# Optimization experiments

Hardware: AMD Instinct MI355X
Metric: run time of the kernel (lower is better)

## Reference

```python
import jax, jax.numpy as jnp
import numpy as np
from math import sqrt

B, S, F, H, FF, L = 16, 512, 512, 8, 2048, 3
HEAD_DIM = F // H
LN_EPS = 1e-5


def setup_inputs() -> dict:
    key = jax.random.key(0)
    ks = iter(jax.random.split(key, 80))

    def nrm(shape, scale=0.02):
        return jax.random.normal(next(ks), shape, jnp.float32) * scale

    inp = {
        "embedding": jax.random.normal(next(ks), (B, S, F), jnp.float32),
        "lengths": jax.random.randint(next(ks), (B,), 1, S + 1, dtype=jnp.int32),
    }
    for p in ("enc", "dec"):
        inp[p + "_wqkv"] = nrm((L, 3, F, F))
        inp[p + "_bqkv"] = nrm((L, 3, F))
        inp[p + "_wo"] = nrm((L, F, F))
        inp[p + "_bo"] = nrm((L, F))
        inp[p + "_ln1_g"] = jnp.ones((L, F), jnp.float32)
        inp[p + "_ln1_b"] = jnp.zeros((L, F), jnp.float32)
        inp[p + "_ff_w1"] = nrm((L, F, FF))
        inp[p + "_ff_b1"] = nrm((L, FF))
        inp[p + "_ff_w2"] = nrm((L, FF, F))
        inp[p + "_ff_b2"] = nrm((L, F))
        inp[p + "_ln2_g"] = jnp.ones((L, F), jnp.float32)
        inp[p + "_ln2_b"] = jnp.zeros((L, F), jnp.float32)
    inp["ptr_w_q"] = nrm((F,), 1.0)
    inp["ptr_w_k"] = nrm((F,), 1.0)
    return inp


def _ln(x, g, b):
    mu = x.mean(-1, keepdims=True)
    var = ((x - mu) ** 2).mean(-1, keepdims=True)
    return (x - mu) / jnp.sqrt(var + LN_EPS) * g + b


def _mha(q_in, kv_in, wqkv, bqkv, wo, bo, mask):
    # q_in [b,sq,f], kv_in [b,sk,f], mask broadcastable to [b,h,sq,sk] (True = masked)
    b, sq, f = q_in.shape
    q = q_in @ wqkv[0] + bqkv[0]
    k = kv_in @ wqkv[1] + bqkv[1]
    v = kv_in @ wqkv[2] + bqkv[2]

    def split(t):
        return t.reshape(t.shape[0], t.shape[1], H, HEAD_DIM).transpose(0, 2, 1, 3)

    q, k, v = split(q), split(k), split(v)  # [b,h,s,dh]
    scores = jnp.einsum("bhqd,bhkd->bhqk", q, k) / sqrt(HEAD_DIM)
    scores = jnp.where(mask, jnp.finfo(scores.dtype).min, scores)
    attn = jax.nn.softmax(scores, axis=-1)
    out = jnp.einsum("bhqk,bhkd->bhqd", attn, v)
    out = out.transpose(0, 2, 1, 3).reshape(b, sq, f)
    return out @ wo + bo


def _layer(x, mem, mask, wqkv, bqkv, wo, bo, ln1_g, ln1_b, w1, b1, w2, b2, ln2_g, ln2_b):
    x = _ln(x + _mha(x, mem, wqkv, bqkv, wo, bo, mask), ln1_g, ln1_b)
    ff = jax.nn.gelu(x @ w1 + b1, approximate=False) @ w2 + b2
    return _ln(x + ff, ln2_g, ln2_b)


def _forward(embedding, lengths,
             enc_wqkv, enc_bqkv, enc_wo, enc_bo, enc_ln1_g, enc_ln1_b,
             enc_ff_w1, enc_ff_b1, enc_ff_w2, enc_ff_b2, enc_ln2_g, enc_ln2_b,
             dec_wqkv, dec_bqkv, dec_wo, dec_bo, dec_ln1_g, dec_ln1_b,
             dec_ff_w1, dec_ff_b1, dec_ff_w2, dec_ff_b2, dec_ln2_g, dec_ln2_b,
             ptr_w_q, ptr_w_k):
    b, s, f = embedding.shape
    pos = jnp.arange(s)
    key_mask = pos[None, :] >= lengths[:, None]  # [b,s] True = padded

    # ---- encoder (self-attn with key padding mask) ----
    enc_mask = key_mask[:, None, None, :]  # [b,1,1,s]
    x = embedding
    for i in range(L):
        x = _layer(x, x, enc_mask,
                   enc_wqkv[i], enc_bqkv[i], enc_wo[i], enc_bo[i],
                   enc_ln1_g[i], enc_ln1_b[i],
                   enc_ff_w1[i], enc_ff_b1[i], enc_ff_w2[i], enc_ff_b2[i],
                   enc_ln2_g[i], enc_ln2_b[i])
    memory = x

    # ---- decoder: all timesteps batched (no recurrent state in original loop) ----
    # query t attends keys j < min(t, len); t=0 is overridden with zeros below
    # (key 0 left unmasked for t=0 only to keep softmax finite).
    t = jnp.arange(s)
    limit = jnp.minimum(jnp.maximum(t, 1)[None, :], lengths[:, None])  # [b,sq]
    dec_mask = (pos[None, None, :] >= limit[:, :, None])[:, None, :, :]  # [b,1,sq,sk]
    y = embedding
    for i in range(L):
        y = _layer(y, memory, dec_mask,
                   dec_wqkv[i], dec_bqkv[i], dec_wo[i], dec_bo[i],
                   dec_ln1_g[i], dec_ln1_b[i],
                   dec_ff_w1[i], dec_ff_b1[i], dec_ff_w2[i], dec_ff_b2[i],
                   dec_ln2_g[i], dec_ln2_b[i])

    # ---- pointer logits ----
    wq = y @ ptr_w_q        # [b, sq]
    wk = memory @ ptr_w_k   # [b, sk]
    ptr = jax.nn.sigmoid((wq[:, None, :] + wk[:, :, None]) / sqrt(f))  # [b, sk, sq]
    return jnp.where(t[None, None, :] == 0, 0.0, ptr)


def reference(embedding, lengths,
              enc_wqkv, enc_bqkv, enc_wo, enc_bo, enc_ln1_g, enc_ln1_b,
              enc_ff_w1, enc_ff_b1, enc_ff_w2, enc_ff_b2, enc_ln2_g, enc_ln2_b,
              dec_wqkv, dec_bqkv, dec_wo, dec_bo, dec_ln1_g, dec_ln1_b,
              dec_ff_w1, dec_ff_b1, dec_ff_w2, dec_ff_b2, dec_ln2_g, dec_ln2_b,
              ptr_w_q, ptr_w_k):
    return _forward(embedding, lengths,
                    enc_wqkv, enc_bqkv, enc_wo, enc_bo, enc_ln1_g, enc_ln1_b,
                    enc_ff_w1, enc_ff_b1, enc_ff_w2, enc_ff_b2, enc_ln2_g, enc_ln2_b,
                    dec_wqkv, dec_bqkv, dec_wo, dec_bo, dec_ln1_g, dec_ln1_b,
                    dec_ff_w1, dec_ff_b1, dec_ff_w2, dec_ff_b2, dec_ln2_g, dec_ln2_b,
                    ptr_w_q, ptr_w_k)
```

## Files before the change

### kernel.cpp

```cpp
#include <hip/hip_runtime.h>
#include <hip/hip_bf16.h>
#include <math.h>

#define TB 16
#define TS 512
#define TF 512
#define TH 8
#define TFF 2048
#define TL 3

typedef unsigned short u16;
typedef short bf16x8 __attribute__((ext_vector_type(8)));
typedef float f32x4 __attribute__((ext_vector_type(4)));

__device__ __forceinline__ u16 f2b(float f) {
    __hip_bfloat16 h = __float2bfloat16(f);
    return *reinterpret_cast<u16*>(&h);
}
__device__ __forceinline__ float b2f(u16 u) {
    unsigned int v = ((unsigned int)u) << 16;
    return __builtin_bit_cast(float, v);
}

__device__ __forceinline__ void gload_lds16(const void* g, void* l) {
    __builtin_amdgcn_global_load_lds(
        (const __attribute__((address_space(1))) unsigned int*)g,
        (__attribute__((address_space(3))) unsigned int*)l, 16, 0, 0);
}

__global__ __launch_bounds__(256) void k_transpose_w(
    const float* __restrict__ src, u16* __restrict__ dst, int K, int N)
{
    __shared__ float tile[32][33];
    const int z = blockIdx.z;
    src += (size_t)z * K * N;
    dst += (size_t)z * K * N;
    const int n0 = blockIdx.x * 32, k0 = blockIdx.y * 32;
    const int tx = threadIdx.x & 31, ty = threadIdx.x >> 5;
    #pragma unroll
    for (int i = 0; i < 32; i += 8)
        tile[ty + i][tx] = src[(size_t)(k0 + ty + i) * N + n0 + tx];
    __syncthreads();
    #pragma unroll
    for (int i = 0; i < 32; i += 8)
        dst[(size_t)(n0 + ty + i) * K + k0 + tx] = f2b(tile[tx][ty + i]);
}

__global__ __launch_bounds__(256) void k_cvt(
    const float* __restrict__ src, u16* __restrict__ d16, int n4)
{
    const int i = blockIdx.x * 256 + threadIdx.x;
    if (i >= n4) return;
    float4 v = ((const float4*)src)[i];
    ushort4 p;
    p.x = f2b(v.x); p.y = f2b(v.y); p.z = f2b(v.z); p.w = f2b(v.w);
    ((ushort4*)d16)[i] = p;
}

template<int EPI, int BM, int BN>
__global__ __launch_bounds__(512, 2) void k_g8(
    const u16* __restrict__ A, const u16* __restrict__ A2, int asplit,
    const u16* __restrict__ BT,
    const float* __restrict__ bias, const u16* __restrict__ residb,
    u16* __restrict__ outb,
    u16* __restrict__ out_k, u16* __restrict__ out_v,
    int N, int K, int ldo, int coloff)
{
    constexpr int WN  = (BM == 256) ? 2 : 4;
    constexpr int CS  = BN / WN;
    constexpr int NFB = CS / 16;
    constexpr int NLA = BM / 64, NLB = BN / 64;
    constexpr int NL  = NLA + NLB;
    __shared__ __align__(16) u16 SH[2 * BM * 64 + 2 * BN * 64];
    u16* Asm = SH;
    u16* Bsm = SH + 2 * BM * 64;

    const int gx = gridDim.x;
    int bid = blockIdx.y * gx + blockIdx.x;
    const int cpx = (gx * gridDim.y) >> 3;
    bid = (bid & 7) * cpx + (bid >> 3);
    const int bn = bid % gx, bm = bid / gx;

    const int t = threadIdx.x;
    const int w = t >> 6, l = t & 63;
    const int wm = w / WN, wn = w % WN;
    const int lhi = l >> 4, llo = l & 15;

    f32x4 acc[4][NFB];
    #pragma unroll
    for (int m = 0; m < 4; ++m)
        #pragma unroll
        for (int n = 0; n < NFB; ++n)
            acc[m][n] = f32x4{0.f, 0.f, 0.f, 0.f};

    const u16* Asrc = (bn * BN < asplit) ? A : A2;
    const int lr = l >> 3;
    const int lcz = ((l & 7) ^ lr) * 8;
    const u16* Ag = Asrc + (size_t)(bm * BM + w * 8 + lr) * K + lcz;
    const u16* Bg = BT + (size_t)(bn * BN + w * 8 + lr) * K + lcz;

    auto stage = [&](int buf, int tt) {
        const int kofs = tt << 6;
        #pragma unroll
        for (int i = 0; i < NLA; ++i)
            gload_lds16(Ag + (size_t)i * 64 * K + kofs,
                        Asm + buf * (BM * 64) + (i * 64 + w * 8) * 64);
        #pragma unroll
        for (int i = 0; i < NLB; ++i)
            gload_lds16(Bg + (size_t)i * 64 * K + kofs,
                        Bsm + buf * (BN * 64) + (i * 64 + w * 8) * 64);
    };

    const int NT = K >> 6;
    stage(0, 0);
    stage(1, 1);
    for (int tt = 0; tt < NT; ++tt) {
        const int cur = tt & 1;
        if (tt + 1 < NT) {
            if constexpr (NL == 8) asm volatile("s_waitcnt vmcnt(8)" ::: "memory");
            else                   asm volatile("s_waitcnt vmcnt(4)" ::: "memory");
        } else {
            asm volatile("s_waitcnt vmcnt(0)" ::: "memory");
        }
        __builtin_amdgcn_s_barrier();
        __builtin_amdgcn_sched_barrier(0);

        const u16* Ab = Asm + cur * (BM * 64);
        const u16* Bb = Bsm + cur * (BN * 64);
        bf16x8 af[4][2], bfr[NFB][2];
        #pragma unroll
        for (int m = 0; m < 4; ++m) {
            const int row = wm * 64 + m * 16 + llo;
            const int x = row & 7;
            af[m][0] = *(const bf16x8*)(Ab + row * 64 + ((lhi) ^ x) * 8);
            af[m][1] = *(const bf16x8*)(Ab + row * 64 + ((4 + lhi) ^ x) * 8);
        }
        #pragma unroll
        for (int n = 0; n < NFB; ++n) {
            const int row = wn * CS + n * 16 + llo;
            const int x = row & 7;
            bfr[n][0] = *(const bf16x8*)(Bb + row * 64 + ((lhi) ^ x) * 8);
            bfr[n][1] = *(const bf16x8*)(Bb + row * 64 + ((4 + lhi) ^ x) * 8);
        }
        asm volatile("s_waitcnt lgkmcnt(0)" ::: "memory");
        __builtin_amdgcn_sched_barrier(0);
        __builtin_amdgcn_s_barrier();
        if (tt + 2 < NT) stage(cur, tt + 2);
        __builtin_amdgcn_s_setprio(1);
        #pragma unroll
        for (int kk = 0; kk < 2; ++kk)
            #pragma unroll
            for (int m = 0; m < 4; ++m)
                #pragma unroll
                for (int n = 0; n < NFB; ++n)
                    acc[m][n] = __builtin_amdgcn_mfma_f32_16x16x32_bf16(
                        af[m][kk], bfr[n][kk], acc[m][n], 0, 0, 0);
        __builtin_amdgcn_s_setprio(0);
        __builtin_amdgcn_sched_barrier(0);
    }

    const int colb = bn * BN + wn * CS;
    const int rowb = bm * BM + wm * 64 + lhi * 4;
    const int c0w = coloff + colb;

    if constexpr (EPI == 3 && BM == 256) {
        if (c0w >= 1024) {
            __builtin_amdgcn_s_barrier();
            u16* tb = SH + w * 8192;
            #pragma unroll
            for (int nh = 0; nh < 2; ++nh) {
                #pragma unroll
                for (int ni = 0; ni < 4; ++ni) {
                    const int n = nh * 4 + ni;
                    const int dl = ni * 16 + llo;
                    const float bv = bias[colb + n * 16 + llo];
                    #pragma unroll
                    for (int m = 0; m < 4; ++m) {
                        ushort4 pk;
                        #pragma unroll
                        for (int r = 0; r < 4; ++r)
                            ((u16*)&pk)[r] = f2b(acc[m][n][r] + bv);
                        const int slc = m * 2 + (lhi >> 1);
                        const int addr = nh * 4096 + dl * 64
                                       + ((slc ^ (dl & 7)) << 3) + ((lhi & 1) << 2);
                        *(ushort4*)(tb + addr) = pk;
                    }
                }
            }
            asm volatile("s_waitcnt lgkmcnt(0)" ::: "memory");
            __builtin_amdgcn_sched_barrier(0);
            const int sbase = bm * BM + wm * 64;
            const int bidx = sbase >> 9;
            const int srem = sbase & 511;
            const int cchunk = l & 7;
            #pragma unroll
            for (int nh = 0; nh < 2; ++nh) {
                const int hh = (((c0w >> 6) + nh) & 7);
                u16* vo = out_v + ((size_t)bidx * 8 + hh) * 32768 + srem;
                #pragma unroll
                for (int rr = 0; rr < 8; ++rr) {
                    const int dl2 = (l >> 3) + rr * 8;
                    const int ch = cchunk ^ (dl2 & 7);
                    bf16x8 vv = *(const bf16x8*)(tb + nh * 4096 + dl2 * 64 + ch * 8);
                    *(bf16x8*)(vo + (size_t)dl2 * 512 + cchunk * 8) = vv;
                }
            }
            return;
        }
    }

    #pragma unroll
    for (int n = 0; n < NFB; ++n) {
        const int col = colb + n * 16 + llo;
        const float bv = bias[col];
        #pragma unroll
        for (int m = 0; m < 4; ++m) {
            const int row = rowb + m * 16;
            if (EPI == 3) {
                float vv[4];
                #pragma unroll
                for (int r = 0; r < 4; ++r) vv[r] = acc[m][n][r] + bv;
                const int c = coloff + col;
                if ((c >> 9) == 0) {
                    #pragma unroll
                    for (int r = 0; r < 4; ++r)
                        outb[(size_t)(row + r) * 512 + c] = f2b(vv[r]);
                } else {
                    const int hh = (c >> 6) & 7, d = c & 63;
                    #pragma unroll
                    for (int r = 0; r < 4; ++r) {
                        const int rr = row + r;
                        out_k[((size_t)(rr >> 9) * 8 + hh) * 32768 + (rr & 511) * 64 + d] = f2b(vv[r]);
                    }
                }
            } else {
                #pragma unroll
                for (int r = 0; r < 4; ++r) {
                    float v = acc[m][n][r] + bv;
                    const size_t off = (size_t)(row + r) * ldo + coloff + col;
                    if (EPI == 0) {
                        outb[off] = f2b(v);
                    } else if (EPI == 1) {
                        v = 0.5f * v * (1.f + erff(v * 0.70710678118654752f));
                        outb[off] = f2b(v);
                    } else {
                        v += b2f(residb[off]);
                        outb[off] = f2b(v);
                    }
                }
            }
        }
    }
}

template<int DEC>
__global__ __launch_bounds__(256) void k_attn(
    const u16* __restrict__ qb, const u16* __restrict__ kc,
    const u16* __restrict__ vtp, const int* __restrict__ lengths,
    u16* __restrict__ out)
{
    __shared__ __align__(16) u16 Ks[2][64 * 64];
    __shared__ __align__(16) u16 Vs[2][64 * 64];
    __shared__ __align__(16) u16 plds[4][16][64];
    __shared__ float alds[4][16];
    __shared__ float llds[4][16];
    const int qt = blockIdx.x;
    const int bh = blockIdx.y;
    const int b = bh >> 3;
    const int h = bh & 7;
    const int t = threadIdx.x, w = t >> 6, l = t & 63;
    const int lhi = l >> 4, llo = l & 15;
    const int len = lengths[b];
    const int qrow0 = qt * 64 + w * 16;
    const int q = qrow0 + llo;

    const u16* qp = qb + (size_t)(b * TS + q) * 512 + h * 64 + lhi * 8;
    bf16x8 qf0 = *(const bf16x8*)(qp);
    bf16x8 qf1 = *(const bf16x8*)(qp + 32);

    const u16* kb = kc  + (size_t)bh * 32768;
    const u16* vb = vtp + (size_t)bh * 32768;

    const int qlim = DEC ? min(max(q, 1), len) : len;
    const int limb = DEC ? min(qt * 64 + 63, len) : len;
    const int ktend = (limb + 63) >> 6;

    f32x4 o[4];
    #pragma unroll
    for (int g = 0; g < 4; ++g) o[g] = f32x4{0.f, 0.f, 0.f, 0.f};
    float mrun = -1e30f, lrun = 0.f;

    const float SC = 0.18033688011112042f;

    const int sr = w * 8 + (l >> 3);
    const int sc = (((l & 7) ^ (sr & 7)) << 3);
    auto stage = [&](int buf, int ktt) {
        gload_lds16(kb + ((ktt * 64 + sr) << 6) + sc,        &Ks[buf][(w * 8) * 64]);
        gload_lds16(kb + ((ktt * 64 + 32 + sr) << 6) + sc,   &Ks[buf][(32 + w * 8) * 64]);
        gload_lds16(vb + (size_t)sr * 512 + ktt * 64 + sc,   &Vs[buf][(w * 8) * 64]);
        gload_lds16(vb + (size_t)(32 + sr) * 512 + ktt * 64 + sc, &Vs[buf][(32 + w * 8) * 64]);
    };

    stage(0, 0);
    for (int kt = 0; kt < ktend; ++kt) {
        const int cur = kt & 1;
        if (kt + 1 < ktend) {
            stage(cur ^ 1, kt + 1);
            asm volatile("s_waitcnt vmcnt(4)" ::: "memory");
        } else {
            asm volatile("s_waitcnt vmcnt(0)" ::: "memory");
        }
        __builtin_amdgcn_s_barrier();
        __builtin_amdgcn_sched_barrier(0);

        bf16x8 kf[4][2], vf[4][2];
        #pragma unroll
        for (int g = 0; g < 4; ++g) {
            const int row = g * 16 + llo;
            const int x = row & 7;
            kf[g][0] = *(const bf16x8*)&Ks[cur][row * 64 + ((lhi) ^ x) * 8];
            kf[g][1] = *(const bf16x8*)&Ks[cur][row * 64 + ((4 + lhi) ^ x) * 8];
            vf[g][0] = *(const bf16x8*)&Vs[cur][row * 64 + ((lhi) ^ x) * 8];
            vf[g][1] = *(const bf16x8*)&Vs[cur][row * 64 + ((4 + lhi) ^ x) * 8];
        }
        f32x4 s[4];
        #pragma unroll
        for (int g = 0; g < 4; ++g) {
            s[g] = f32x4{0.f, 0.f, 0.f, 0.f};
            s[g] = __builtin_amdgcn_mfma_f32_16x16x32_bf16(kf[g][0], qf0, s[g], 0, 0, 0);
            s[g] = __builtin_amdgcn_mfma_f32_16x16x32_bf16(kf[g][1], qf1, s[g], 0, 0, 0);
        }
        #pragma unroll
        for (int g = 0; g < 4; ++g) {
            const int key = kt * 64 + g * 16 + lhi * 4;
            #pragma unroll
            for (int r = 0; r < 4; ++r)
                s[g][r] = (key + r < qlim) ? s[g][r] * SC : -1e30f;
        }
        float tm = fmaxf(fmaxf(fmaxf(s[0][0], s[0][1]), fmaxf(s[0][2], s[0][3])),
                         fmaxf(fmaxf(s[1][0], s[1][1]), fmaxf(s[1][2], s[1][3])));
        tm = fmaxf(tm, fmaxf(fmaxf(fmaxf(s[2][0], s[2][1]), fmaxf(s[2][2], s[2][3])),
                             fmaxf(fmaxf(s[3][0], s[3][1]), fmaxf(s[3][2], s[3][3]))));
        tm = fmaxf(tm, __shfl_xor(tm, 16));
        tm = fmaxf(tm, __shfl_xor(tm, 32));
        const float mnew = fmaxf(mrun, tm);
        const float alpha = exp2f(mrun - mnew);
        mrun = mnew;
        float rs = 0.f;
        ushort4 pk[4];
        #pragma unroll
        for (int g = 0; g < 4; ++g) {
            #pragma unroll
            for (int r = 0; r < 4; ++r) {
                const float p = exp2f(s[g][r] - mnew);
                rs += p;
                ((u16*)&pk[g])[r] = f2b(p);
            }
        }
        rs += __shfl_xor(rs, 16);
        rs += __shfl_xor(rs, 32);
        lrun = lrun * alpha + rs;
        if (lhi == 0) alds[w][llo] = alpha;
        #pragma unroll
        for (int g = 0; g < 4; ++g) {
            const int chw = (g * 2 + (lhi >> 1)) ^ (llo & 7);
            *(ushort4*)((char*)&plds[w][0][0] + llo * 128 + chw * 16 + (lhi & 1) * 8) = pk[g];
        }
        const float4 av = *(const float4*)&alds[w][lhi * 4];
        #pragma unroll
        for (int g = 0; g < 4; ++g) {
            o[g][0] *= av.x; o[g][1] *= av.y; o[g][2] *= av.z; o[g][3] *= av.w;
        }
        #pragma unroll
        for (int ks = 0; ks < 2; ++ks) {
            const int chr = (ks * 4 + lhi) ^ (llo & 7);
            bf16x8 pa = *(const bf16x8*)((const char*)&plds[w][0][0] + llo * 128 + chr * 16);
            #pragma unroll
            for (int g = 0; g < 4; ++g)
                o[g] = __builtin_amdgcn_mfma_f32_16x16x32_bf16(pa, vf[g][ks], o[g], 0, 0, 0);
        }
        __builtin_amdgcn_sched_barrier(0);
        __builtin_amdgcn_s_barrier();
    }

    if (lhi == 0) llds[w][llo] = 1.f / lrun;
    __builtin_amdgcn_s_waitcnt(0);
    const float4 linv = *(const float4*)&llds[w][lhi * 4];
    #pragma unroll
    for (int g = 0; g < 4; ++g) {
        const int d = h * 64 + g * 16 + llo;
        #pragma unroll
        for (int r = 0; r < 4; ++r) {
            const int qq = qrow0 + lhi * 4 + r;
            out[(size_t)(b * TS + qq) * 512 + d] = f2b(o[g][r] * ((const float*)&linv)[r]);
        }
    }
}

__global__ __launch_bounds__(256) void k_ln(
    const u16* __restrict__ in, const float* __restrict__ gam,
    const float* __restrict__ bet, u16* __restrict__ o16,
    const float* __restrict__ dotv, float* __restrict__ dotout)
{
    const int row = blockIdx.x * 4 + (threadIdx.x >> 6);
    const int l = threadIdx.x & 63;
    bf16x8 vin = *(const bf16x8*)(in + (size_t)row * 512 + l * 8);
    float x[8];
    #pragma unroll
    for (int i = 0; i < 8; ++i) x[i] = b2f((u16)vin[i]);
    float s = x[0] + x[1] + x[2] + x[3] + x[4] + x[5] + x[6] + x[7];
    #pragma unroll
    for (int off = 32; off; off >>= 1) s += __shfl_xor(s, off);
    const float mu = s * (1.f / 512.f);
    float v = 0.f;
    #pragma unroll
    for (int i = 0; i < 8; ++i) { const float d = x[i] - mu; v += d * d; }
    #pragma unroll
    for (int off = 32; off; off >>= 1) v += __shfl_xor(v, off);
    const float rstd = rsqrtf(v * (1.f / 512.f) + 1e-5f);
    float gg[8], bb[8];
    *(float4*)&gg[0] = *(const float4*)(gam + l * 8);
    *(float4*)&gg[4] = *(const float4*)(gam + l * 8 + 4);
    *(float4*)&bb[0] = *(const float4*)(bet + l * 8);
    *(float4*)&bb[4] = *(const float4*)(bet + l * 8 + 4);
    float y[8];
    #pragma unroll
    for (int i = 0; i < 8; ++i) y[i] = (x[i] - mu) * rstd * gg[i] + bb[i];
    ushort4 pk0, pk1;
    pk0.x = f2b(y[0]); pk0.y = f2b(y[1]); pk0.z = f2b(y[2]); pk0.w = f2b(y[3]);
    pk1.x = f2b(y[4]); pk1.y = f2b(y[5]); pk1.z = f2b(y[6]); pk1.w = f2b(y[7]);
    ushort4* o16p = (ushort4*)(o16 + (size_t)row * 512 + l * 8);
    o16p[0] = pk0; o16p[1] = pk1;
    if (dotv) {
        float wa[8];
        *(float4*)&wa[0] = *(const float4*)(dotv + l * 8);
        *(float4*)&wa[4] = *(const float4*)(dotv + l * 8 + 4);
        float ds = 0.f;
        #pragma unroll
        for (int i = 0; i < 8; ++i) ds += y[i] * wa[i];
        #pragma unroll
        for (int off = 32; off; off >>= 1) ds += __shfl_xor(ds, off);
        if (l == 0) dotout[row] = ds;
    }
}

__global__ __launch_bounds__(256) void k_ptr_out(
    const float* __restrict__ wq, const float* __restrict__ wk, float* __restrict__ out)
{
    const int bi = blockIdx.x;
    const int b = bi >> 9;
    const float wki = wk[bi];
    #pragma unroll
    for (int j = threadIdx.x; j < 512; j += 256) {
        float r = 0.f;
        if (j != 0) {
            const float z = (wq[b * 512 + j] + wki) * 0.044194173824159216f;
            r = 1.f / (1.f + __expf(-z));
        }
        out[(size_t)bi * 512 + j] = r;
    }
}

extern "C" void kernel_launch(void* const* d_in, const int* in_sizes, int n_in,
                              void* d_out, int out_size, void* d_ws, size_t ws_size,
                              hipStream_t stream)
{
    const float* emb = (const float*)d_in[0];
    const int* lengths = (const int*)d_in[1];
    struct Pw {
        const float *wqkv, *bqkv, *wo, *bo, *ln1g, *ln1b, *w1, *b1, *w2, *b2, *ln2g, *ln2b;
    } pp[2];
    for (int p = 0; p < 2; ++p) {
        const int base = 2 + p * 12;
        pp[p].wqkv = (const float*)d_in[base + 0];
        pp[p].bqkv = (const float*)d_in[base + 1];
        pp[p].wo   = (const float*)d_in[base + 2];
        pp[p].bo   = (const float*)d_in[base + 3];
        pp[p].ln1g = (const float*)d_in[base + 4];
        pp[p].ln1b = (const float*)d_in[base + 5];
        pp[p].w1   = (const float*)d_in[base + 6];
        pp[p].b1   = (const float*)d_in[base + 7];
        pp[p].w2   = (const float*)d_in[base + 8];
        pp[p].b2   = (const float*)d_in[base + 9];
        pp[p].ln2g = (const float*)d_in[base + 10];
        pp[p].ln2b = (const float*)d_in[base + 11];
    }
    const float* pwq = (const float*)d_in[26];
    const float* pwk = (const float*)d_in[27];

    char* ws = (char*)d_ws;
    auto alloc = [&](size_t bytes) {
        char* p = ws;
        ws += (bytes + 255) & ~(size_t)255;
        return p;
    };
    u16* wqkvT[2], *woT[2], *w1T[2], *w2T[2];
    for (int p = 0; p < 2; ++p) {
        wqkvT[p] = (u16*)alloc((size_t)TL * 1536 * 512 * 2);
        woT[p]   = (u16*)alloc((size_t)TL * 512 * 512 * 2);
        w1T[p]   = (u16*)alloc((size_t)TL * 2048 * 512 * 2);
        w2T[p]   = (u16*)alloc((size_t)TL * 512 * 2048 * 2);
    }
    const size_t MR = (size_t)TB * TS;
    u16*   emb16 = (u16*)alloc(MR * 512 * 2);
    u16*   x16   = (u16*)alloc(MR * 512 * 2);
    u16*   mem16 = (u16*)alloc(MR * 512 * 2);
    u16*   pre16 = (u16*)alloc(MR * 512 * 2);
    u16*   qbuf  = (u16*)alloc(MR * 512 * 2);
    u16*   kcb   = (u16*)alloc((size_t)TB * TH * 512 * 64 * 2);
    u16*   vtb   = (u16*)alloc((size_t)TB * TH * 64 * 512 * 2);
    u16*   att16 = (u16*)alloc(MR * 512 * 2);
    u16*   h16   = (u16*)alloc(MR * 2048 * 2);
    float* wqb   = (float*)alloc(MR * 4);
    float* wkb   = (float*)alloc(MR * 4);

    for (int p = 0; p < 2; ++p) {
        k_transpose_w<<<dim3(16, 16, 9), 256, 0, stream>>>(pp[p].wqkv, wqkvT[p], 512, 512);
        k_transpose_w<<<dim3(16, 16, 3), 256, 0, stream>>>(pp[p].wo, woT[p], 512, 512);
        k_transpose_w<<<dim3(64, 16, 3), 256, 0, stream>>>(pp[p].w1, w1T[p], 512, 2048);
        k_transpose_w<<<dim3(16, 64, 3), 256, 0, stream>>>(pp[p].w2, w2T[p], 2048, 512);
    }

    const int n4 = (int)(MR * 512 / 4);
    k_cvt<<<4096, 256, 0, stream>>>(emb, emb16, n4);

    for (int i = 0; i < TL; ++i) {
        const u16* xin = (i == 0) ? emb16 : x16;
        k_g8<3, 256, 256><<<dim3(6, 32), 512, 0, stream>>>(
            xin, xin, 1536, wqkvT[0] + (size_t)i * 1536 * 512, pp[0].bqkv + i * 1536,
            nullptr, qbuf, kcb, vtb, 1536, 512, 1536, 0);
        k_attn<0><<<dim3(8, 128), 256, 0, stream>>>(qbuf, kcb, vtb, lengths, att16);
        k_g8<2, 128, 128><<<dim3(4, 64), 512, 0, stream>>>(
            att16, att16, 512, woT[0] + (size_t)i * 512 * 512, pp[0].bo + i * 512,
            xin, pre16, nullptr, nullptr, 512, 512, 512, 0);
        k_ln<<<2048, 256, 0, stream>>>(pre16, pp[0].ln1g + i * 512, pp[0].ln1b + i * 512,
                                       x16, nullptr, nullptr);
        k_g8<1, 256, 256><<<dim3(8, 32), 512, 0, stream>>>(
            x16, x16, 2048, w1T[0] + (size_t)i * 2048 * 512, pp[0].b1 + i * 2048,
            nullptr, h16, nullptr, nullptr, 2048, 512, 2048, 0);
        k_g8<2, 128, 128><<<dim3(4, 64), 512, 0, stream>>>(
            h16, h16, 512, w2T[0] + (size_t)i * 512 * 2048, pp[0].b2 + i * 512,
            x16, pre16, nullptr, nullptr, 512, 2048, 512, 0);
        if (i == TL - 1)
            k_ln<<<2048, 256, 0, stream>>>(pre16, pp[0].ln2g + i * 512, pp[0].ln2b + i * 512,
                                           mem16, pwk, wkb);
        else
            k_ln<<<2048, 256, 0, stream>>>(pre16, pp[0].ln2g + i * 512, pp[0].ln2b + i * 512,
                                           x16, nullptr, nullptr);
    }

    for (int i = 0; i < TL; ++i) {
        const u16* yin = (i == 0) ? emb16 : x16;
        k_g8<3, 256, 256><<<dim3(6, 32), 512, 0, stream>>>(
            yin, mem16, 512, wqkvT[1] + (size_t)i * 1536 * 512, pp[1].bqkv + i * 1536,
            nullptr, qbuf, kcb, vtb, 1536, 512, 1536, 0);
        k_attn<1><<<dim3(8, 128), 256, 0, stream>>>(qbuf, kcb, vtb, lengths, att16);
        k_g8<2, 128, 128><<<dim3(4, 64), 512, 0, stream>>>(
            att16, att16, 512, woT[1] + (size_t)i * 512 * 512, pp[1].bo + i * 512,
            yin, pre16, nullptr, nullptr, 512, 512, 512, 0);
        k_ln<<<2048, 256, 0, stream>>>(pre16, pp[1].ln1g + i * 512, pp[1].ln1b + i * 512,
                                       x16, nullptr, nullptr);
        k_g8<1, 256, 256><<<dim3(8, 32), 512, 0, stream>>>(
            x16, x16, 2048, w1T[1] + (size_t)i * 2048 * 512, pp[1].b1 + i * 2048,
            nullptr, h16, nullptr, nullptr, 2048, 512, 2048, 0);
        k_g8<2, 128, 128><<<dim3(4, 64), 512, 0, stream>>>(
            h16, h16, 512, w2T[1] + (size_t)i * 512 * 2048, pp[1].b2 + i * 512,
            x16, pre16, nullptr, nullptr, 512, 2048, 512, 0);
        if (i == TL - 1)
            k_ln<<<2048, 256, 0, stream>>>(pre16, pp[1].ln2g + i * 512, pp[1].ln2b + i * 512,
                                           x16, pwq, wqb);
        else
            k_ln<<<2048, 256, 0, stream>>>(pre16, pp[1].ln2g + i * 512, pp[1].ln2b + i * 512,
                                           x16, nullptr, nullptr);
    }

    k_ptr_out<<<TB * TS, 256, 0, stream>>>(wqb, wkb, (float*)d_out);
}
```

Before: 836.5 us.

## Add K=512 GEMM kernel with full A panel resident in LDS

Adds a new GEMM kernel k_gp for the K=512 projections (QKV, output projection, FF1). Each block loads an entire 128x512 A panel into LDS once and streams B fragments straight from global memory into registers, with no double-buffered staging or per-step barriers. This targets the per-k-tile barrier and LDS staging overhead. In exchange, B is read without LDS reuse across waves, occupancy drops to one block per CU, and the global-load latency of B is no longer hidden by an async pipeline.

```diff
diff --git a/kernel.cpp b/kernel.cpp
--- a/kernel.cpp
+++ b/kernel.cpp
@@ -57,23 +57,19 @@
     ((ushort4*)d16)[i] = p;
 }
 
-template<int EPI, int BM, int BN>
-__global__ __launch_bounds__(512, 2) void k_g8(
+template<int EPI, int BN>
+__global__ __launch_bounds__(512, 1) void k_gp(
     const u16* __restrict__ A, const u16* __restrict__ A2, int asplit,
     const u16* __restrict__ BT,
     const float* __restrict__ bias, const u16* __restrict__ residb,
     u16* __restrict__ outb,
     u16* __restrict__ out_k, u16* __restrict__ out_v,
-    int N, int K, int ldo, int coloff)
-{
-    constexpr int WN  = (BM == 256) ? 2 : 4;
-    constexpr int CS  = BN / WN;
+    int N, int ldo, int coloff)
+{
+    constexpr int K = 512;
+    constexpr int CS = BN / 4;
     constexpr int NFB = CS / 16;
-    constexpr int NLA = BM / 64, NLB = BN / 64;
-    constexpr int NL  = NLA + NLB;
-    __shared__ __align__(16) u16 SH[2 * BM * 64 + 2 * BN * 64];
-    u16* Asm = SH;
-    u16* Bsm = SH + 2 * BM * 64;
+    __shared__ __align__(16) u16 Asm[128 * 512];
 
     const int gx = gridDim.x;
     int bid = blockIdx.y * gx + blockIdx.x;
@@ -83,8 +79,20 @@
 
     const int t = threadIdx.x;
     const int w = t >> 6, l = t & 63;
-    const int wm = w / WN, wn = w % WN;
+    const int wm = w >> 2, wn = w & 3;
     const int lhi = l >> 4, llo = l & 15;
+
+    const u16* Asrc = (bn * BN < asplit) ? A : A2;
+    const u16* Ablk = Asrc + (size_t)(bm * 128) * K;
+
+    #pragma unroll
+    for (int j = 0; j < 16; ++j) {
+        const int row = w * 16 + j;
+        const int sch = l ^ (row & 7);
+        gload_lds16(Ablk + (size_t)row * K + sch * 8, Asm + row * 512);
+    }
+    asm volatile("s_waitcnt vmcnt(0)" ::: "memory");
+    __syncthreads();
 
     f32x4 acc[4][NFB];
     #pragma unroll
@@ -93,60 +101,27 @@
         for (int n = 0; n < NFB; ++n)
             acc[m][n] = f32x4{0.f, 0.f, 0.f, 0.f};
 
-    const u16* Asrc = (bn * BN < asplit) ? A : A2;
-    const int lr = l >> 3;
-    const int lcz = ((l & 7) ^ lr) * 8;
-    const u16* Ag = Asrc + (size_t)(bm * BM + w * 8 + lr) * K + lcz;
-    const u16* Bg = BT + (size_t)(bn * BN + w * 8 + lr) * K + lcz;
-
-    auto stage = [&](int buf, int tt) {
-        const int kofs = tt << 6;
-        #pragma unroll
-        for (int i = 0; i < NLA; ++i)
-            gload_lds16(Ag + (size_t)i * 64 * K + kofs,
-                        Asm + buf * (BM * 64) + (i * 64 + w * 8) * 64);
-        #pragma unroll
-        for (int i = 0; i < NLB; ++i)
-            gload_lds16(Bg + (size_t)i * 64 * K + kofs,
-                        Bsm + buf * (BN * 64) + (i * 64 + w * 8) * 64);
-    };
-
-    const int NT = K >> 6;
-    stage(0, 0);
-    stage(1, 1);
-    for (int tt = 0; tt < NT; ++tt) {
-        const int cur = tt & 1;
-        if (tt + 1 < NT) {
-            if constexpr (NL == 8) asm volatile("s_waitcnt vmcnt(8)" ::: "memory");
-            else                   asm volatile("s_waitcnt vmcnt(4)" ::: "memory");
-        } else {
-            asm volatile("s_waitcnt vmcnt(0)" ::: "memory");
-        }
-        __builtin_amdgcn_s_barrier();
-        __builtin_amdgcn_sched_barrier(0);
-
-        const u16* Ab = Asm + cur * (BM * 64);
-        const u16* Bb = Bsm + cur * (BN * 64);
-        bf16x8 af[4][2], bfr[NFB][2];
+    const int colb = bn * BN + wn * CS;
+    const u16* Bbase = BT + (size_t)(colb + llo) * K + lhi * 8;
+
+    #pragma unroll 2
+    for (int tt = 0; tt < 8; ++tt) {
+        bf16x8 bfr[NFB][2];
+        #pragma unroll
+        for (int n = 0; n < NFB; ++n) {
+            const u16* bp = Bbase + (size_t)(n * 16) * K + tt * 64;
+            bfr[n][0] = *(const bf16x8*)(bp);
+            bfr[n][1] = *(const bf16x8*)(bp + 32);
+        }
+        bf16x8 af[4][2];
         #pragma unroll
         for (int m = 0; m < 4; ++m) {
             const int row = wm * 64 + m * 16 + llo;
             const int x = row & 7;
-            af[m][0] = *(const bf16x8*)(Ab + row * 64 + ((lhi) ^ x) * 8);
-            af[m][1] = *(const bf16x8*)(Ab + row * 64 + ((4 + lhi) ^ x) * 8);
-        }
-        #pragma unroll
-        for (int n = 0; n < NFB; ++n) {
-            const int row = wn * CS + n * 16 + llo;
-            const int x = row & 7;
-            bfr[n][0] = *(const bf16x8*)(Bb + row * 64 + ((lhi) ^ x) * 8);
-            bfr[n][1] = *(const bf16x8*)(Bb + row * 64 + ((4 + lhi) ^ x) * 8);
-        }
-        asm volatile("s_waitcnt lgkmcnt(0)" ::: "memory");
-        __builtin_amdgcn_sched_barrier(0);
-        __builtin_amdgcn_s_barrier();
-        if (tt + 2 < NT) stage(cur, tt + 2);
-        __builtin_amdgcn_s_setprio(1);
+            const int c0 = tt * 8 + lhi;
+            af[m][0] = *(const bf16x8*)(Asm + row * 512 + ((c0) ^ x) * 8);
+            af[m][1] = *(const bf16x8*)(Asm + row * 512 + ((c0 + 4) ^ x) * 8);
+        }
         #pragma unroll
         for (int kk = 0; kk < 2; ++kk)
             #pragma unroll
@@ -155,55 +130,44 @@
                 for (int n = 0; n < NFB; ++n)
                     acc[m][n] = __builtin_amdgcn_mfma_f32_16x16x32_bf16(
                         af[m][kk], bfr[n][kk], acc[m][n], 0, 0, 0);
-        __builtin_amdgcn_s_setprio(0);
-        __builtin_amdgcn_sched_barrier(0);
-    }
-
-    const int colb = bn * BN + wn * CS;
-    const int rowb = bm * BM + wm * 64 + lhi * 4;
+    }
+
+    const int rowb = bm * 128 + wm * 64 + lhi * 4;
     const int c0w = coloff + colb;
 
-    if constexpr (EPI == 3 && BM == 256) {
+    if constexpr (EPI == 3 && BN == 256) {
         if (c0w >= 1024) {
-            __builtin_amdgcn_s_barrier();
-            u16* tb = SH + w * 8192;
-            #pragma unroll
-            for (int nh = 0; nh < 2; ++nh) {
+            __syncthreads();
+            u16* tb = Asm + w * 4096;
+            #pragma unroll
+            for (int n = 0; n < 4; ++n) {
+                const int dl = n * 16 + llo;
+                const float bv = bias[colb + n * 16 + llo];
                 #pragma unroll
-                for (int ni = 0; ni < 4; ++ni) {
-                    const int n = nh * 4 + ni;
-                    const int dl = ni * 16 + llo;
-                    const float bv = bias[colb + n * 16 + llo];
+                for (int m = 0; m < 4; ++m) {
+                    ushort4 pk;
                     #pragma unroll
-                    for (int m = 0; m < 4; ++m) {
-                        ushort4 pk;
-                        #pragma unroll
-                        for (int r = 0; r < 4; ++r)
-                            ((u16*)&pk)[r] = f2b(acc[m][n][r] + bv);
-                        const int slc = m * 2 + (lhi >> 1);
-                        const int addr = nh * 4096 + dl * 64
-                                       + ((slc ^ (dl & 7)) << 3) + ((lhi & 1) << 2);
-                        *(ushort4*)(tb + addr) = pk;
-                    }
+                    for (int r = 0; r < 4; ++r)
+                        ((u16*)&pk)[r] = f2b(acc[m][n][r] + bv);
+                    const int slc = m * 2 + (lhi >> 1);
+                    const int addr = dl * 64 + ((slc ^ (dl & 7)) << 3) + ((lhi & 1) << 2);
+                    *(ushort4*)(tb + addr) = pk;
                 }
             }
             asm volatile("s_waitcnt lgkmcnt(0)" ::: "memory");
             __builtin_amdgcn_sched_barrier(0);
-            const int sbase = bm * BM + wm * 64;
+            const int sbase = bm * 128 + wm * 64;
             const int bidx = sbase >> 9;
             const int srem = sbase & 511;
+            const int hh = (c0w >> 6) & 7;
+            u16* vo = out_v + ((size_t)bidx * 8 + hh) * 32768 + srem;
             const int cchunk = l & 7;
             #pragma unroll
-            for (int nh = 0; nh < 2; ++nh) {
-                const int hh = (((c0w >> 6) + nh) & 7);
-                u16* vo = out_v + ((size_t)bidx * 8 + hh) * 32768 + srem;
-                #pragma unroll
-                for (int rr = 0; rr < 8; ++rr) {
-                    const int dl2 = (l >> 3) + rr * 8;
-                    const int ch = cchunk ^ (dl2 & 7);
-                    bf16x8 vv = *(const bf16x8*)(tb + nh * 4096 + dl2 * 64 + ch * 8);
-                    *(bf16x8*)(vo + (size_t)dl2 * 512 + cchunk * 8) = vv;
-                }
+            for (int rr = 0; rr < 8; ++rr) {
+                const int dl2 = (l >> 3) + rr * 8;
+                const int ch = cchunk ^ (dl2 & 7);
+                bf16x8 vv = *(const bf16x8*)(tb + dl2 * 64 + ch * 8);
+                *(bf16x8*)(vo + (size_t)dl2 * 512 + cchunk * 8) = vv;
             }
             return;
         }
@@ -238,15 +202,140 @@
                 for (int r = 0; r < 4; ++r) {
                     float v = acc[m][n][r] + bv;
                     const size_t off = (size_t)(row + r) * ldo + coloff + col;
-                    if (EPI == 0) {
-                        outb[off] = f2b(v);
-                    } else if (EPI == 1) {
+                    if (EPI == 1) {
                         v = 0.5f * v * (1.f + erff(v * 0.70710678118654752f));
                         outb[off] = f2b(v);
                     } else {
                         v += b2f(residb[off]);
                         outb[off] = f2b(v);
                     }
+                }
+            }
+        }
+    }
+}
+
+template<int EPI, int BM, int BN>
+__global__ __launch_bounds__(512, 2) void k_g8(
+    const u16* __restrict__ A, const u16* __restrict__ A2, int asplit,
+    const u16* __restrict__ BT,
+    const float* __restrict__ bias, const u16* __restrict__ residb,
+    u16* __restrict__ outb,
+    u16* __restrict__ out_k, u16* __restrict__ out_v,
+    int N, int K, int ldo, int coloff)
+{
+    constexpr int WN  = (BM == 256) ? 2 : 4;
+    constexpr int CS  = BN / WN;
+    constexpr int NFB = CS / 16;
+    constexpr int NLA = BM / 64, NLB = BN / 64;
+    constexpr int NL  = NLA + NLB;
+    __shared__ __align__(16) u16 SH[2 * BM * 64 + 2 * BN * 64];
+    u16* Asm = SH;
+    u16* Bsm = SH + 2 * BM * 64;
+
+    const int gx = gridDim.x;
+    int bid = blockIdx.y * gx + blockIdx.x;
+    const int cpx = (gx * gridDim.y) >> 3;
+    bid = (bid & 7) * cpx + (bid >> 3);
+    const int bn = bid % gx, bm = bid / gx;
+
+    const int t = threadIdx.x;
+    const int w = t >> 6, l = t & 63;
+    const int wm = w / WN, wn = w % WN;
+    const int lhi = l >> 4, llo = l & 15;
+
+    f32x4 acc[4][NFB];
+    #pragma unroll
+    for (int m = 0; m < 4; ++m)
+        #pragma unroll
+        for (int n = 0; n < NFB; ++n)
+            acc[m][n] = f32x4{0.f, 0.f, 0.f, 0.f};
+
+    const u16* Asrc = (bn * BN < asplit) ? A : A2;
+    const int lr = l >> 3;
+    const int lcz = ((l & 7) ^ lr) * 8;
+    const u16* Ag = Asrc + (size_t)(bm * BM + w * 8 + lr) * K + lcz;
+    const u16* Bg = BT + (size_t)(bn * BN + w * 8 + lr) * K + lcz;
+
+    auto stage = [&](int buf, int tt) {
+        const int kofs = tt << 6;
+        #pragma unroll
+        for (int i = 0; i < NLA; ++i)
+            gload_lds16(Ag + (size_t)i * 64 * K + kofs,
+                        Asm + buf * (BM * 64) + (i * 64 + w * 8) * 64);
+        #pragma unroll
+        for (int i = 0; i < NLB; ++i)
+            gload_lds16(Bg + (size_t)i * 64 * K + kofs,
+                        Bsm + buf * (BN * 64) + (i * 64 + w * 8) * 64);
+    };
+
+    const int NT = K >> 6;
+    stage(0, 0);
+    stage(1, 1);
+    for (int tt = 0; tt < NT; ++tt) {
+        const int cur = tt & 1;
+        if (tt + 1 < NT) {
+            if constexpr (NL == 8) asm volatile("s_waitcnt vmcnt(8)" ::: "memory");
+            else                   asm volatile("s_waitcnt vmcnt(4)" ::: "memory");
+        } else {
+            asm volatile("s_waitcnt vmcnt(0)" ::: "memory");
+        }
+        __builtin_amdgcn_s_barrier();
+        __builtin_amdgcn_sched_barrier(0);
+
+        const u16* Ab = Asm + cur * (BM * 64);
+        const u16* Bb = Bsm + cur * (BN * 64);
+        bf16x8 af[4][2], bfr[NFB][2];
+        #pragma unroll
+        for (int m = 0; m < 4; ++m) {
+            const int row = wm * 64 + m * 16 + llo;
+            const int x = row & 7;
+            af[m][0] = *(const bf16x8*)(Ab + row * 64 + ((lhi) ^ x) * 8);
+            af[m][1] = *(const bf16x8*)(Ab + row * 64 + ((4 + lhi) ^ x) * 8);
+        }
+        #pragma unroll
+        for (int n = 0; n < NFB; ++n) {
+            const int row = wn * CS + n * 16 + llo;
+            const int x = row & 7;
+            bfr[n][0] = *(const bf16x8*)(Bb + row * 64 + ((lhi) ^ x) * 8);
+            bfr[n][1] = *(const bf16x8*)(Bb + row * 64 + ((4 + lhi) ^ x) * 8);
+        }
+        asm volatile("s_waitcnt lgkmcnt(0)" ::: "memory");
+        __builtin_amdgcn_sched_barrier(0);
+        __builtin_amdgcn_s_barrier();
+        if (tt + 2 < NT) stage(cur, tt + 2);
+        __builtin_amdgcn_s_setprio(1);
+        #pragma unroll
+        for (int kk = 0; kk < 2; ++kk)
+            #pragma unroll
+            for (int m = 0; m < 4; ++m)
+                #pragma unroll
+                for (int n = 0; n < NFB; ++n)
+                    acc[m][n] = __builtin_amdgcn_mfma_f32_16x16x32_bf16(
+                        af[m][kk], bfr[n][kk], acc[m][n], 0, 0, 0);
+        __builtin_amdgcn_s_setprio(0);
+        __builtin_amdgcn_sched_barrier(0);
+    }
+
+    const int colb = bn * BN + wn * CS;
+    const int rowb = bm * BM + wm * 64 + lhi * 4;
+    #pragma unroll
+    for (int n = 0; n < NFB; ++n) {
+        const int col = colb + n * 16 + llo;
+        const float bv = bias[col];
+        #pragma unroll
+        for (int m = 0; m < 4; ++m) {
+            const int row = rowb + m * 16;
+            #pragma unroll
+            for (int r = 0; r < 4; ++r) {
+                float v = acc[m][n][r] + bv;
+                const size_t off = (size_t)(row + r) * ldo + coloff + col;
+                if (EPI == 1) {
+                    v = 0.5f * v * (1.f + erff(v * 0.70710678118654752f));
+                    outb[off] = f2b(v);
+                } else {
+                    v += b2f(residb[off]);
+                    outb[off] = f2b(v);
                 }
             }
         }
@@ -526,18 +615,18 @@
 
     for (int i = 0; i < TL; ++i) {
         const u16* xin = (i == 0) ? emb16 : x16;
-        k_g8<3, 256, 256><<<dim3(6, 32), 512, 0, stream>>>(
+        k_gp<3, 256><<<dim3(6, 64), 512, 0, stream>>>(
             xin, xin, 1536, wqkvT[0] + (size_t)i * 1536 * 512, pp[0].bqkv + i * 1536,
-            nullptr, qbuf, kcb, vtb, 1536, 512, 1536, 0);
+            nullptr, qbuf, kcb, vtb, 1536, 1536, 0);
         k_attn<0><<<dim3(8, 128), 256, 0, stream>>>(qbuf, kcb, vtb, lengths, att16);
-        k_g8<2, 128, 128><<<dim3(4, 64), 512, 0, stream>>>(
+        k_gp<2, 128><<<dim3(4, 64), 512, 0, stream>>>(
             att16, att16, 512, woT[0] + (size_t)i * 512 * 512, pp[0].bo + i * 512,
-            xin, pre16, nullptr, nullptr, 512, 512, 512, 0);
+            xin, pre16, nullptr, nullptr, 512, 512, 0);
         k_ln<<<2048, 256, 0, stream>>>(pre16, pp[0].ln1g + i * 512, pp[0].ln1b + i * 512,
                                        x16, nullptr, nullptr);
-        k_g8<1, 256, 256><<<dim3(8, 32), 512, 0, stream>>>(
+        k_gp<1, 256><<<dim3(8, 64), 512, 0, stream>>>(
             x16, x16, 2048, w1T[0] + (size_t)i * 2048 * 512, pp[0].b1 + i * 2048,
-            nullptr, h16, nullptr, nullptr, 2048, 512, 2048, 0);
+            nullptr, h16, nullptr, nullptr, 2048, 2048, 0);
         k_g8<2, 128, 128><<<dim3(4, 64), 512, 0, stream>>>(
             h16, h16, 512, w2T[0] + (size_t)i * 512 * 2048, pp[0].b2 + i * 512,
             x16, pre16, nullptr, nullptr, 512, 2048, 512, 0);
@@ -551,18 +640,18 @@
 
     for (int i = 0; i < TL; ++i) {
         const u16* yin = (i == 0) ? emb16 : x16;
-        k_g8<3, 256, 256><<<dim3(6, 32), 512, 0, stream>>>(
+        k_gp<3, 256><<<dim3(6, 64), 512, 0, stream>>>(
             yin, mem16, 512, wqkvT[1] + (size_t)i * 1536 * 512, pp[1].bqkv + i * 1536,
-            nullptr, qbuf, kcb, vtb, 1536, 512, 1536, 0);
+            nullptr, qbuf, kcb, vtb, 1536, 1536, 0);
         k_attn<1><<<dim3(8, 128), 256, 0, stream>>>(qbuf, kcb, vtb, lengths, att16);
-        k_g8<2, 128, 128><<<dim3(4, 64), 512, 0, stream>>>(
+        k_gp<2, 128><<<dim3(4, 64), 512, 0, stream>>>(
             att16, att16, 512, woT[1] + (size_t)i * 512 * 512, pp[1].bo + i * 512,
-            yin, pre16, nullptr, nullptr, 512, 512, 512, 0);
+            yin, pre16, nullptr, nullptr, 512, 512, 0);
         k_ln<<<2048, 256, 0, stream>>>(pre16, pp[1].ln1g + i * 512, pp[1].ln1b + i * 512,
                                        x16, nullptr, nullptr);
-        k_g8<1, 256, 256><<<dim3(8, 32), 512, 0, stream>>>(
+        k_gp<1, 256><<<dim3(8, 64), 512, 0, stream>>>(
             x16, x16, 2048, w1T[1] + (size_t)i * 2048 * 512, pp[1].b1 + i * 2048,
-            nullptr, h16, nullptr, nullptr, 2048, 512, 2048, 0);
+            nullptr, h16, nullptr, nullptr, 2048, 2048, 0);
         k_g8<2, 128, 128><<<dim3(4, 64), 512, 0, stream>>>(
             h16, h16, 512, w2T[1] + (size_t)i * 512 * 2048, pp[1].b2 + i * 512,
             x16, pre16, nullptr, nullptr, 512, 2048, 512, 0);
```

Result: slower. 1.059 ms (+26.6%).
